# Kernel optimization log

Hardware: AMD Instinct MI355X
Metric: run time of the kernel (lower is better)

Reference implementation:

```python
import jax, jax.numpy as jnp
import numpy as np

B, T, C, H, M, MEM_FREQ = 1, 2048, 768, 12, 64, 64


def setup_inputs() -> dict:
    key = jax.random.key(0)
    k1, k2, k3 = jax.random.split(key, 3)
    x = jax.random.normal(k1, (B, T, C), jnp.float32)
    # landmark ('mem') token every MEM_FREQ positions, as in landmark-attention data prep
    is_mem = jnp.broadcast_to((jnp.arange(T) % MEM_FREQ == MEM_FREQ - 1)[None, :], (B, T))
    w_qkv = 0.02 * jax.random.normal(k2, (C, 3 * C), jnp.float32)
    b_qkv = jnp.zeros((3 * C,), jnp.float32)
    w_proj = 0.02 * jax.random.normal(k3, (C, C), jnp.float32)
    b_proj = jnp.zeros((C,), jnp.float32)
    return {"x": x, "is_mem": is_mem, "w_qkv": w_qkv, "b_qkv": b_qkv,
            "w_proj": w_proj, "b_proj": b_proj}


def _grouped_softmax(att, im, mask, last_sec):
    """LandmarkGroupedSoftmaxFunction + landmark_grouped_softmax (eval, no dropout).
    att/im/mask/last_sec: (B,H,T,T); softmax over last dim grouped into M buckets."""
    neg = -jnp.inf
    last_and_rest = last_sec | mask
    full_access = im | last_and_rest
    mem_group_idx = jnp.cumsum(im.astype(jnp.int32), axis=-1)  # (B,H,T,T)
    resp = jnp.where(last_and_rest | im, M - 1, mem_group_idx)  # bucket id per key

    R = att.shape[0] * att.shape[1] * att.shape[2]
    Tk = att.shape[3]
    xf = att.reshape(R, Tk)
    idxf = resp.reshape(R, Tk)

    row_max = jax.vmap(lambda xr, ir: jnp.full((M,), neg, xr.dtype).at[ir].max(xr))
    row_sum = jax.vmap(lambda xr, ir: jnp.zeros((M,), xr.dtype).at[ir].add(xr))

    max_by_group = row_max(xf, idxf)                                   # (R,M)
    maxes = jnp.take_along_axis(max_by_group, idxf, axis=-1)
    safe_max = jnp.where(jnp.isinf(maxes), 0.0, maxes)
    x_exp = jnp.exp(xf - safe_max)
    denom_g = row_sum(x_exp, idxf)
    denom = jnp.take_along_axis(denom_g, idxf, axis=-1)
    small = denom < 0.5
    probs = jnp.where(small, 0.0, x_exp / jnp.where(small, 1.0, denom))

    imf = im.reshape(R, Tk)
    lsf = last_sec.reshape(R, Tk)
    faf = full_access.reshape(R, Tk)
    # group_prob[g] = prob of landmark g; last slot = mass of last (current) section
    gp_idx = jnp.where(imf, mem_group_idx.reshape(R, Tk) - 1, M - 1)
    group_prob = row_sum(jnp.where(imf, probs, 0.0), gp_idx)
    group_prob = group_prob.at[:, M - 1].set(jnp.sum(probs * lsf, axis=-1))
    gathered = jnp.take_along_axis(group_prob, idxf, axis=-1)
    mult = jnp.where(faf, lsf.astype(probs.dtype), gathered)
    return (probs * mult).reshape(att.shape)


def reference(x, is_mem, w_qkv, b_qkv, w_proj, b_proj):
    Bx, Tx, Cx = x.shape
    hd = Cx // H
    qkv = x @ w_qkv + b_qkv
    q, k, v = jnp.split(qkv, 3, axis=-1)
    q = q.reshape(Bx, Tx, H, hd).transpose(0, 2, 1, 3)  # (B,H,T,hd)
    k = k.reshape(Bx, Tx, H, hd).transpose(0, 2, 1, 3)
    v = v.reshape(Bx, Tx, H, hd).transpose(0, 2, 1, 3)

    att = jnp.einsum('bhqd,bhkd->bhqk', q, k) * (1.0 / np.sqrt(hd))
    causal = jnp.triu(jnp.ones((Tx, Tx), bool), 1)[None, None]  # True = masked
    att = jnp.where(causal, -jnp.inf, att)

    im = jnp.broadcast_to(is_mem[:, None, None, :], (Bx, H, Tx, Tx))
    im_i = im.astype(jnp.int32)
    mem_ids = jnp.where(causal, 0, jnp.cumsum(im_i, axis=-1) - im_i)
    last_sec = mem_ids == jnp.max(mem_ids, axis=-1, keepdims=True)
    mask = causal | (im & last_sec)   # landmarks of the current section are masked
    last_sec = last_sec & ~mask
    im = im & ~mask
    att = jnp.where(mask, -jnp.inf, att)

    probs = _grouped_softmax(att, im, mask, last_sec)
    y = jnp.einsum('bhqk,bhkd->bhqd', probs, v)
    y = y.transpose(0, 2, 1, 3).reshape(Bx, Tx, Cx)
    return y @ w_proj + b_proj
```

## Files before the change

kernel.cpp:

```cpp
#include <hip/hip_runtime.h>
#include <hip/hip_bf16.h>
#include <math.h>

#define TT 2048
#define CC 768
#define NH 12
#define HDIM 64
#define QKVLD 2304
#define NSEC 32
#define NCHMAX 8

typedef short bf16x8 __attribute__((ext_vector_type(8)));
typedef float f32x4 __attribute__((ext_vector_type(4)));

#define MFMA16(a, b, c) __builtin_amdgcn_mfma_f32_16x16x32_bf16(a, b, c, 0, 0, 0)

__device__ __forceinline__ ushort f2bf(float f) {
  __hip_bfloat16 h = __float2bfloat16(f);
  return *reinterpret_cast<ushort*>(&h);
}

__device__ __forceinline__ float bf2f(ushort u) {
  __hip_bfloat16 b = *reinterpret_cast<__hip_bfloat16*>(&u);
  return __bfloat162float(b);
}

__device__ __forceinline__ void gload_lds16(const ushort* g, ushort* l) {
  __builtin_amdgcn_global_load_lds(
      (const __attribute__((address_space(1))) void*)g,
      (__attribute__((address_space(3))) void*)l, 16, 0, 0);
}

__device__ __forceinline__ int chunk_base(int q) {
  const int a = q >> 2, b = q & 3;
  return q + 2 * a * (a - 1) + a * b;
}

__global__ __launch_bounds__(256) void convert_bf16_kernel(
    const float* __restrict__ in, ushort* __restrict__ out, int n) {
  int i = (blockIdx.x * 256 + threadIdx.x) * 8;
  if (i >= n) return;
  float4 a = *(const float4*)&in[i];
  float4 b = *(const float4*)&in[i + 4];
  bf16x8 o;
  o[0] = (short)f2bf(a.x); o[1] = (short)f2bf(a.y);
  o[2] = (short)f2bf(a.z); o[3] = (short)f2bf(a.w);
  o[4] = (short)f2bf(b.x); o[5] = (short)f2bf(b.y);
  o[6] = (short)f2bf(b.z); o[7] = (short)f2bf(b.w);
  *(bf16x8*)&out[i] = o;
}

__global__ __launch_bounds__(256) void transpose2_kernel(
    const float* __restrict__ w_qkv, const float* __restrict__ w_proj,
    ushort* __restrict__ wqkvT, ushort* __restrict__ wprojT) {
  const int z = blockIdx.z;
  const float* in = z ? w_proj : w_qkv;
  ushort* out = z ? wprojT : wqkvT;
  const int N = z ? CC : QKVLD;
  const int K = CC;
  if (blockIdx.x * 64 >= N) return;

  __shared__ float tile[64][65];
  const int t = threadIdx.x;
  const int kb = blockIdx.y * 64, nb = blockIdx.x * 64;
  const int rg = t >> 4, cg = t & 15;
#pragma unroll
  for (int r = 0; r < 4; ++r) {
    float4 v = *(const float4*)&in[(size_t)(kb + rg * 4 + r) * N + nb + cg * 4];
    tile[rg * 4 + r][cg * 4 + 0] = v.x;
    tile[rg * 4 + r][cg * 4 + 1] = v.y;
    tile[rg * 4 + r][cg * 4 + 2] = v.z;
    tile[rg * 4 + r][cg * 4 + 3] = v.w;
  }
  __syncthreads();
#pragma unroll
  for (int r = 0; r < 4; ++r) {
    const int nl = rg * 4 + r;
    ushort4 o;
    o.x = f2bf(tile[cg * 4 + 0][nl]);
    o.y = f2bf(tile[cg * 4 + 1][nl]);
    o.z = f2bf(tile[cg * 4 + 2][nl]);
    o.w = f2bf(tile[cg * 4 + 3][nl]);
    *(ushort4*)&out[(size_t)(nb + nl) * K + kb + cg * 4] = o;
  }
}

__global__ __launch_bounds__(256) void gemm_bt_bf16_kernel(
    const ushort* __restrict__ A, const ushort* __restrict__ Bt,
    const float* __restrict__ bias,
    ushort* __restrict__ qkvb, ushort* __restrict__ vT,
    float* __restrict__ Cf,
    int M, int N, int K) {
  __shared__ ushort As[64 * 64];
  __shared__ ushort Bs[64 * 64];
  const int tid = threadIdx.x;
  const int wid = tid >> 6, lane = tid & 63;
  const int lr = lane & 15, lg = lane >> 4;
  const int wr = wid >> 1, wc = wid & 1;
  const int bm = blockIdx.y * 64, bn = blockIdx.x * 64;

  f32x4 acc[2][2];
#pragma unroll
  for (int m = 0; m < 2; ++m)
#pragma unroll
    for (int n = 0; n < 2; ++n) acc[m][n] = (f32x4){0.f, 0.f, 0.f, 0.f};

  const int srow = lane >> 3;
  const int scol = (lane & 7) * 8;

  for (int k0 = 0; k0 < K; k0 += 64) {
    __syncthreads();
#pragma unroll
    for (int half = 0; half < 2; ++half) {
      const int row = half * 32 + wid * 8 + srow;
      gload_lds16(A  + (size_t)(bm + row) * K + k0 + scol,
                  &As[(half * 32 + wid * 8) * 64]);
      gload_lds16(Bt + (size_t)(bn + row) * K + k0 + scol,
                  &Bs[(half * 32 + wid * 8) * 64]);
    }
    __syncthreads();
#pragma unroll
    for (int kk = 0; kk < 2; ++kk) {
      bf16x8 af[2], bfr[2];
#pragma unroll
      for (int m = 0; m < 2; ++m)
        af[m] = *(const bf16x8*)&As[(wr * 32 + m * 16 + lr) * 64 + kk * 32 + lg * 8];
#pragma unroll
      for (int n = 0; n < 2; ++n)
        bfr[n] = *(const bf16x8*)&Bs[(wc * 32 + n * 16 + lr) * 64 + kk * 32 + lg * 8];
#pragma unroll
      for (int m = 0; m < 2; ++m)
#pragma unroll
        for (int n = 0; n < 2; ++n)
          acc[m][n] = MFMA16(af[m], bfr[n], acc[m][n]);
    }
  }

  float bb[2];
#pragma unroll
  for (int n = 0; n < 2; ++n) bb[n] = bias[bn + wc * 32 + n * 16 + lr];

  if (Cf) {
#pragma unroll
    for (int m = 0; m < 2; ++m)
#pragma unroll
      for (int n = 0; n < 2; ++n)
#pragma unroll
        for (int r = 0; r < 4; ++r) {
          const int row = bm + wr * 32 + m * 16 + lg * 4 + r;
          const int col = bn + wc * 32 + n * 16 + lr;
          Cf[(size_t)row * N + col] = acc[m][n][r] + bb[n];
        }
  } else if (bn < 768) {
#pragma unroll
    for (int m = 0; m < 2; ++m)
#pragma unroll
      for (int n = 0; n < 2; ++n)
#pragma unroll
        for (int r = 0; r < 4; ++r) {
          const int row = bm + wr * 32 + m * 16 + lg * 4 + r;
          const int col = bn + wc * 32 + n * 16 + lr;
          qkvb[(size_t)row * QKVLD + col] = f2bf((acc[m][n][r] + bb[n]) * 0.125f);
        }
  } else if (bn < 1536) {
#pragma unroll
    for (int m = 0; m < 2; ++m)
#pragma unroll
      for (int n = 0; n < 2; ++n)
#pragma unroll
        for (int r = 0; r < 4; ++r) {
          const int row = bm + wr * 32 + m * 16 + lg * 4 + r;
          const int col = bn + wc * 32 + n * 16 + lr;
          qkvb[(size_t)row * QKVLD + col] = f2bf(acc[m][n][r] + bb[n]);
        }
  } else {
#pragma unroll
    for (int m = 0; m < 2; ++m)
#pragma unroll
      for (int n = 0; n < 2; ++n) {
        const int row0 = bm + wr * 32 + m * 16 + lg * 4;
        const int vrow = bn + wc * 32 + n * 16 + lr - 1536;
        ushort4 o;
        o.x = f2bf(acc[m][n][0] + bb[n]);
        o.y = f2bf(acc[m][n][1] + bb[n]);
        o.z = f2bf(acc[m][n][2] + bb[n]);
        o.w = f2bf(acc[m][n][3] + bb[n]);
        *(ushort4*)&vT[(size_t)vrow * TT + row0] = o;
      }
  }
}

__global__ __launch_bounds__(256) void attn_chunk_kernel(
    const ushort* __restrict__ qkvb,
    const ushort* __restrict__ vT,
    ushort* __restrict__ pacc,
    float* __restrict__ pstats) {
  const int c = blockIdx.x, qsec = blockIdx.y, h = blockIdx.z;
  if (c * 4 > qsec) return;
  const int tid = threadIdx.x;
  const int wid = tid >> 6, lane = tid & 63;
  const int lr = lane & 15, lg = lane >> 4;

  __shared__ ushort Kl[64][72];
  __shared__ ushort Vl[64][72];
  __shared__ ushort Pl[4][16][72];

  const int qloc = wid * 16 + lr;
  const ushort* qp = qkvb + (size_t)(qsec * 64 + qloc) * QKVLD + h * HDIM + lg * 8;
  const bf16x8 qf0 = *(const bf16x8*)qp;
  const bf16x8 qf1 = *(const bf16x8*)(qp + 32);

  f32x4 accy[4];
#pragma unroll
  for (int nt = 0; nt < 4; ++nt) accy[nt] = (f32x4){0.f, 0.f, 0.f, 0.f};
  float mrun = -INFINITY, dl = 0.f;

  const int s0 = c * 4;
  const int send = (s0 + 3 < qsec) ? s0 + 3 : qsec;

  const int srow = tid >> 2, scol = (tid & 3) * 16;
  const ushort* kbase = qkvb + (size_t)srow * QKVLD + CC + h * HDIM + scol;
  const ushort* vbase = vT + (size_t)(h * HDIM + srow) * TT + scol;

  bf16x8 kr0, kr1, vr0, vr1;
  {
    const ushort* kp = kbase + (size_t)s0 * 64 * QKVLD;
    kr0 = *(const bf16x8*)kp; kr1 = *(const bf16x8*)(kp + 8);
    const ushort* vp = vbase + s0 * 64;
    vr0 = *(const bf16x8*)vp; vr1 = *(const bf16x8*)(vp + 8);
  }

  for (int s = s0; s <= send; ++s) {
    __syncthreads();
    *(bf16x8*)&Kl[srow][scol]     = kr0;
    *(bf16x8*)&Kl[srow][scol + 8] = kr1;
    *(bf16x8*)&Vl[srow][scol]     = vr0;
    *(bf16x8*)&Vl[srow][scol + 8] = vr1;
    bf16x8 nk0, nk1, nv0, nv1;
    if (s < send) {
      const ushort* kp = kbase + (size_t)(s + 1) * 64 * QKVLD;
      nk0 = *(const bf16x8*)kp; nk1 = *(const bf16x8*)(kp + 8);
      const ushort* vp = vbase + (s + 1) * 64;
      nv0 = *(const bf16x8*)vp; nv1 = *(const bf16x8*)(vp + 8);
    }
    __syncthreads();

    f32x4 sacc[4];
#pragma unroll
    for (int nt = 0; nt < 4; ++nt) sacc[nt] = (f32x4){0.f, 0.f, 0.f, 0.f};
#pragma unroll
    for (int nt = 0; nt < 4; ++nt) {
      bf16x8 kf0 = *(const bf16x8*)&Kl[nt * 16 + lr][lg * 8];
      bf16x8 kf1 = *(const bf16x8*)&Kl[nt * 16 + lr][32 + lg * 8];
      sacc[nt] = MFMA16(kf0, qf0, sacc[nt]);
      sacc[nt] = MFMA16(kf1, qf1, sacc[nt]);
    }

    const bool curq = (s == qsec);
    float lmv = 0.f;
    if (!curq) {
      lmv = __shfl(sacc[3][3], 48 + lr);
      if (lg == 3) sacc[3][3] = -INFINITY;
    } else {
      const int lim = qloc < 62 ? qloc : 62;
#pragma unroll
      for (int nt = 0; nt < 4; ++nt)
#pragma unroll
        for (int r = 0; r < 4; ++r)
          if (nt * 16 + lg * 4 + r > lim) sacc[nt][r] = -INFINITY;
    }

    float vmax = sacc[0][0];
#pragma unroll
    for (int nt = 0; nt < 4; ++nt)
#pragma unroll
      for (int r = 0; r < 4; ++r) vmax = fmaxf(vmax, sacc[nt][r]);
    vmax = fmaxf(vmax, __shfl_xor(vmax, 16));
    vmax = fmaxf(vmax, __shfl_xor(vmax, 32));

    float base_;
    if (curq) {
      float mn = fmaxf(mrun, vmax);
      float sc = __expf(mrun - mn);
#pragma unroll
      for (int nt = 0; nt < 4; ++nt) accy[nt] *= sc;
      dl *= sc; mrun = mn; base_ = mn;
    } else {
      base_ = vmax;
    }

    float ssum = 0.f;
#pragma unroll
    for (int nt = 0; nt < 4; ++nt)
#pragma unroll
      for (int r = 0; r < 4; ++r) {
        sacc[nt][r] = __expf(sacc[nt][r] - base_);
        ssum += sacc[nt][r];
      }
    ssum += __shfl_xor(ssum, 16);
    ssum += __shfl_xor(ssum, 32);

    float coef;
    if (!curq) {
      float mn = fmaxf(mrun, lmv);
      float sc = __expf(mrun - mn);
      float el = __expf(lmv - mn);
#pragma unroll
      for (int nt = 0; nt < 4; ++nt) accy[nt] *= sc;
      dl = dl * sc + el; mrun = mn;
      coef = el / ssum;
    } else {
      coef = 1.f;
      dl += ssum;
    }

#pragma unroll
    for (int nt = 0; nt < 4; ++nt) {
      ushort4 o;
      o.x = f2bf(sacc[nt][0] * coef);
      o.y = f2bf(sacc[nt][1] * coef);
      o.z = f2bf(sacc[nt][2] * coef);
      o.w = f2bf(sacc[nt][3] * coef);
      *(ushort4*)&Pl[wid][lr][nt * 16 + lg * 4] = o;
    }

    {
      bf16x8 pf0 = *(const bf16x8*)&Pl[wid][lr][lg * 8];
      bf16x8 pf1 = *(const bf16x8*)&Pl[wid][lr][32 + lg * 8];
#pragma unroll
      for (int nt = 0; nt < 4; ++nt) {
        bf16x8 vf0 = *(const bf16x8*)&Vl[nt * 16 + lr][lg * 8];
        bf16x8 vf1 = *(const bf16x8*)&Vl[nt * 16 + lr][32 + lg * 8];
        accy[nt] = MFMA16(vf0, pf0, accy[nt]);
        accy[nt] = MFMA16(vf1, pf1, accy[nt]);
      }
    }

    if (s < send) { kr0 = nk0; kr1 = nk1; vr0 = nv0; vr1 = nv1; }
  }

  const int slot = (chunk_base(qsec) + c) * NH + h;
  ushort* ap = pacc + (size_t)slot * 4096;
#pragma unroll
  for (int nt = 0; nt < 4; ++nt)
#pragma unroll
    for (int r = 0; r < 4; ++r)
      ap[(nt * 16 + lg * 4 + r) * 64 + wid * 16 + lr] = f2bf(accy[nt][r]);
  if (lg == 0) {
    float* st = pstats + (size_t)slot * 128;
    st[(wid * 16 + lr) * 2 + 0] = mrun;
    st[(wid * 16 + lr) * 2 + 1] = dl;
  }
}

__global__ __launch_bounds__(256) void attn_merge_kernel(
    const ushort* __restrict__ pacc, const float* __restrict__ pstats,
    ushort* __restrict__ y) {
  const int qsec = blockIdx.x, h = blockIdx.y;
  const int tid = threadIdx.x;
  const int w = tid >> 6, q = tid & 63;
  const int nch = (qsec >> 2) + 1;
  const int sbase = chunk_base(qsec);
  __shared__ float Lt[64][65];

  float M = -INFINITY;
  for (int cc = 0; cc < nch; ++cc)
    M = fmaxf(M, pstats[(size_t)((sbase + cc) * NH + h) * 128 + q * 2]);
  float D = 0.f;
  for (int cc = 0; cc < nch; ++cc) {
    const float* st = pstats + (size_t)((sbase + cc) * NH + h) * 128 + q * 2;
    D += __expf(st[0] - M) * st[1];
  }
  const float invD = 1.f / D;

  float val[16];
#pragma unroll
  for (int j = 0; j < 16; ++j) val[j] = 0.f;
  for (int cc = 0; cc < nch; ++cc) {
    const int slot = (sbase + cc) * NH + h;
    const float cw = __expf(pstats[(size_t)slot * 128 + q * 2] - M) * invD;
    const ushort* ap = pacc + (size_t)slot * 4096 + w * 16 * 64 + q;
#pragma unroll
    for (int j = 0; j < 16; ++j) val[j] += cw * bf2f(ap[j * 64]);
  }
#pragma unroll
  for (int j = 0; j < 16; ++j) Lt[w * 16 + j][q] = val[j];
  __syncthreads();

  const int d = tid & 63;
#pragma unroll
  for (int j = 0; j < 16; ++j) {
    const int qq = w * 16 + j;
    y[(size_t)(qsec * 64 + qq) * CC + h * HDIM + d] = f2bf(Lt[d][qq]);
  }
}

extern "C" void kernel_launch(void* const* d_in, const int* in_sizes, int n_in,
                              void* d_out, int out_size, void* d_ws, size_t ws_size,
                              hipStream_t stream) {
  const float* x      = (const float*)d_in[0];
  const float* w_qkv  = (const float*)d_in[2];
  const float* b_qkv  = (const float*)d_in[3];
  const float* w_proj = (const float*)d_in[4];
  const float* b_proj = (const float*)d_in[5];
  float* out = (float*)d_out;

  ushort* wprojT = (ushort*)d_ws;
  ushort* qkvb   = wprojT + (size_t)CC * CC;
  ushort* vT     = qkvb + (size_t)TT * QKVLD;
  ushort* y      = vT + (size_t)CC * TT;
  ushort* pacc   = y + (size_t)TT * CC;
  float*  pstats = (float*)(pacc + (size_t)1728 * 4096);
  ushort* xb     = pacc;
  ushort* wqkvT  = xb + (size_t)TT * CC;

  convert_bf16_kernel<<<TT * CC / (256 * 8), 256, 0, stream>>>(x, xb, TT * CC);
  transpose2_kernel<<<dim3(QKVLD / 64, CC / 64, 2), 256, 0, stream>>>(
      w_qkv, w_proj, wqkvT, wprojT);

  gemm_bt_bf16_kernel<<<dim3(QKVLD / 64, TT / 64), 256, 0, stream>>>(
      xb, wqkvT, b_qkv, qkvb, vT, nullptr, TT, QKVLD, CC);

  attn_chunk_kernel<<<dim3(NCHMAX, NSEC, NH), 256, 0, stream>>>(
      qkvb, vT, pacc, pstats);
  attn_merge_kernel<<<dim3(NSEC, NH), 256, 0, stream>>>(pacc, pstats, y);

  gemm_bt_bf16_kernel<<<dim3(CC / 64, TT / 64), 256, 0, stream>>>(
      y, wprojT, b_proj, nullptr, nullptr, out, TT, CC, CC);
}
```

Baseline: 86.16 us.

## XOR-swizzle LDS tiles and use direct global-to-LDS loads in attention

The GEMM and attention chunk kernels now store their 64-wide bf16 tiles in LDS with an XOR swizzle on 16-byte column groups instead of padded rows, which is meant to avoid bank conflicts on the MFMA fragment reads. The attention kernel drops its register-staged prefetch of K and V and instead issues direct global-to-LDS loads each step, and it gets a launch-bounds occupancy hint of 8 blocks. The direct loads remove register pressure and staging copies but lose the overlap of next-tile loads with compute, so load latency may become exposed.

Measured after the change: 79.81 us. 1.08x faster.

```diff
diff --git a/kernel.cpp b/kernel.cpp
--- a/kernel.cpp
+++ b/kernel.cpp
@@ -105,17 +105,18 @@
 #pragma unroll
     for (int n = 0; n < 2; ++n) acc[m][n] = (f32x4){0.f, 0.f, 0.f, 0.f};
 
-  const int srow = lane >> 3;
-  const int scol = (lane & 7) * 8;
+  const int srow7 = lane >> 3;
+  const int scolw = ((lane & 7) ^ srow7) * 8;
+  const int rswz = lr & 7;
 
   for (int k0 = 0; k0 < K; k0 += 64) {
     __syncthreads();
 #pragma unroll
     for (int half = 0; half < 2; ++half) {
-      const int row = half * 32 + wid * 8 + srow;
-      gload_lds16(A  + (size_t)(bm + row) * K + k0 + scol,
+      const int row = half * 32 + wid * 8 + srow7;
+      gload_lds16(A  + (size_t)(bm + row) * K + k0 + scolw,
                   &As[(half * 32 + wid * 8) * 64]);
-      gload_lds16(Bt + (size_t)(bn + row) * K + k0 + scol,
+      gload_lds16(Bt + (size_t)(bn + row) * K + k0 + scolw,
                   &Bs[(half * 32 + wid * 8) * 64]);
     }
     __syncthreads();
@@ -124,10 +125,12 @@
       bf16x8 af[2], bfr[2];
 #pragma unroll
       for (int m = 0; m < 2; ++m)
-        af[m] = *(const bf16x8*)&As[(wr * 32 + m * 16 + lr) * 64 + kk * 32 + lg * 8];
+        af[m] = *(const bf16x8*)
+            &As[(wr * 32 + m * 16 + lr) * 64 + (((kk * 4 + lg) ^ rswz) * 8)];
 #pragma unroll
       for (int n = 0; n < 2; ++n)
-        bfr[n] = *(const bf16x8*)&Bs[(wc * 32 + n * 16 + lr) * 64 + kk * 32 + lg * 8];
+        bfr[n] = *(const bf16x8*)
+            &Bs[(wc * 32 + n * 16 + lr) * 64 + (((kk * 4 + lg) ^ rswz) * 8)];
 #pragma unroll
       for (int m = 0; m < 2; ++m)
 #pragma unroll
@@ -190,7 +193,7 @@
   }
 }
 
-__global__ __launch_bounds__(256) void attn_chunk_kernel(
+__global__ __launch_bounds__(256, 8) void attn_chunk_kernel(
     const ushort* __restrict__ qkvb,
     const ushort* __restrict__ vT,
     ushort* __restrict__ pacc,
@@ -201,9 +204,9 @@
   const int wid = tid >> 6, lane = tid & 63;
   const int lr = lane & 15, lg = lane >> 4;
 
-  __shared__ ushort Kl[64][72];
-  __shared__ ushort Vl[64][72];
-  __shared__ ushort Pl[4][16][72];
+  __shared__ ushort Kl[64 * 64];
+  __shared__ ushort Vl[64 * 64];
+  __shared__ ushort Pl[4 * 16 * 64];
 
   const int qloc = wid * 16 + lr;
   const ushort* qp = qkvb + (size_t)(qsec * 64 + qloc) * QKVLD + h * HDIM + lg * 8;
@@ -218,31 +221,22 @@
   const int s0 = c * 4;
   const int send = (s0 + 3 < qsec) ? s0 + 3 : qsec;
 
-  const int srow = tid >> 2, scol = (tid & 3) * 16;
-  const ushort* kbase = qkvb + (size_t)srow * QKVLD + CC + h * HDIM + scol;
-  const ushort* vbase = vT + (size_t)(h * HDIM + srow) * TT + scol;
-
-  bf16x8 kr0, kr1, vr0, vr1;
-  {
-    const ushort* kp = kbase + (size_t)s0 * 64 * QKVLD;
-    kr0 = *(const bf16x8*)kp; kr1 = *(const bf16x8*)(kp + 8);
-    const ushort* vp = vbase + s0 * 64;
-    vr0 = *(const bf16x8*)vp; vr1 = *(const bf16x8*)(vp + 8);
-  }
+  const int srow = wid * 8 + (lane >> 3);
+  const int scolw = ((lane & 7) ^ (lane >> 3)) * 8;
+  const ushort* ksrc = qkvb + (size_t)(s0 * 64 + srow) * QKVLD + CC + h * HDIM + scolw;
+  const ushort* vsrc = vT + (size_t)(h * HDIM + srow) * TT + s0 * 64 + scolw;
+  ushort* kdst = &Kl[wid * 512];
+  ushort* vdst = &Vl[wid * 512];
+  const int rswz = lr & 7;
 
   for (int s = s0; s <= send; ++s) {
     __syncthreads();
-    *(bf16x8*)&Kl[srow][scol]     = kr0;
-    *(bf16x8*)&Kl[srow][scol + 8] = kr1;
-    *(bf16x8*)&Vl[srow][scol]     = vr0;
-    *(bf16x8*)&Vl[srow][scol + 8] = vr1;
-    bf16x8 nk0, nk1, nv0, nv1;
-    if (s < send) {
-      const ushort* kp = kbase + (size_t)(s + 1) * 64 * QKVLD;
-      nk0 = *(const bf16x8*)kp; nk1 = *(const bf16x8*)(kp + 8);
-      const ushort* vp = vbase + (s + 1) * 64;
-      nv0 = *(const bf16x8*)vp; nv1 = *(const bf16x8*)(vp + 8);
-    }
+    gload_lds16(ksrc,                          kdst);
+    gload_lds16(ksrc + (size_t)32 * QKVLD,     kdst + 2048);
+    gload_lds16(vsrc,                          vdst);
+    gload_lds16(vsrc + (size_t)32 * TT,        vdst + 2048);
+    ksrc += (size_t)64 * QKVLD;
+    vsrc += 64;
     __syncthreads();
 
     f32x4 sacc[4];
@@ -250,8 +244,8 @@
     for (int nt = 0; nt < 4; ++nt) sacc[nt] = (f32x4){0.f, 0.f, 0.f, 0.f};
 #pragma unroll
     for (int nt = 0; nt < 4; ++nt) {
-      bf16x8 kf0 = *(const bf16x8*)&Kl[nt * 16 + lr][lg * 8];
-      bf16x8 kf1 = *(const bf16x8*)&Kl[nt * 16 + lr][32 + lg * 8];
+      bf16x8 kf0 = *(const bf16x8*)&Kl[(nt * 16 + lr) * 64 + ((lg ^ rswz) * 8)];
+      bf16x8 kf1 = *(const bf16x8*)&Kl[(nt * 16 + lr) * 64 + (((4 + lg) ^ rswz) * 8)];
       sacc[nt] = MFMA16(kf0, qf0, sacc[nt]);
       sacc[nt] = MFMA16(kf1, qf1, sacc[nt]);
     }
@@ -314,29 +308,28 @@
       dl += ssum;
     }
 
-#pragma unroll
-    for (int nt = 0; nt < 4; ++nt) {
-      ushort4 o;
-      o.x = f2bf(sacc[nt][0] * coef);
-      o.y = f2bf(sacc[nt][1] * coef);
-      o.z = f2bf(sacc[nt][2] * coef);
-      o.w = f2bf(sacc[nt][3] * coef);
-      *(ushort4*)&Pl[wid][lr][nt * 16 + lg * 4] = o;
-    }
-
     {
-      bf16x8 pf0 = *(const bf16x8*)&Pl[wid][lr][lg * 8];
-      bf16x8 pf1 = *(const bf16x8*)&Pl[wid][lr][32 + lg * 8];
+      ushort* prow = &Pl[wid * 1024 + lr * 64];
 #pragma unroll
       for (int nt = 0; nt < 4; ++nt) {
-        bf16x8 vf0 = *(const bf16x8*)&Vl[nt * 16 + lr][lg * 8];
-        bf16x8 vf1 = *(const bf16x8*)&Vl[nt * 16 + lr][32 + lg * 8];
+        ushort4 o;
+        o.x = f2bf(sacc[nt][0] * coef);
+        o.y = f2bf(sacc[nt][1] * coef);
+        o.z = f2bf(sacc[nt][2] * coef);
+        o.w = f2bf(sacc[nt][3] * coef);
+        *(ushort4*)&prow[(((nt * 2 + (lg >> 1)) ^ rswz) * 8) + (lg & 1) * 4] = o;
+      }
+
+      bf16x8 pf0 = *(const bf16x8*)&prow[(lg ^ rswz) * 8];
+      bf16x8 pf1 = *(const bf16x8*)&prow[((4 + lg) ^ rswz) * 8];
+#pragma unroll
+      for (int nt = 0; nt < 4; ++nt) {
+        bf16x8 vf0 = *(const bf16x8*)&Vl[(nt * 16 + lr) * 64 + ((lg ^ rswz) * 8)];
+        bf16x8 vf1 = *(const bf16x8*)&Vl[(nt * 16 + lr) * 64 + (((4 + lg) ^ rswz) * 8)];
         accy[nt] = MFMA16(vf0, pf0, accy[nt]);
         accy[nt] = MFMA16(vf1, pf1, accy[nt]);
       }
     }
-
-    if (s < send) { kr0 = nk0; kr1 = nk1; vr0 = nv0; vr1 = nv1; }
   }
 
   const int slot = (chunk_base(qsec) + c) * NH + h;
```
